# Kernel tuning notes

Hardware: AMD Instinct MI355X
Metric: run time of the kernel (lower is better)

Reference implementation:

```python
import jax, jax.numpy as jnp
import numpy as np

D_MODEL = 1024
N_HEADS = 16
D_K = D_MODEL // N_HEADS


def _xavier(key, shape):
    fan_in, fan_out = shape[1], shape[0]
    a = np.sqrt(6.0 / (fan_in + fan_out))
    return jax.random.uniform(key, shape, jnp.float32, -a, a)


def setup_inputs() -> dict:
    key = jax.random.key(0)
    kx, kq, kk, kv, ko = jax.random.split(key, 5)
    x = jax.random.normal(kx, (2, 2048, D_MODEL), jnp.float32)
    # nn.Linear weights are [out, in]; y = x @ W.T
    Wq = _xavier(kq, (D_MODEL, D_MODEL))
    Wk = _xavier(kk, (D_MODEL, D_MODEL))
    Wv = _xavier(kv, (D_MODEL, D_MODEL))
    Wo = _xavier(ko, (D_MODEL, D_MODEL))
    bo = jnp.zeros((D_MODEL,), jnp.float32)
    return {"x": x, "Wq": Wq, "Wk": Wk, "Wv": Wv, "Wo": Wo, "bo": bo}


def reference(x, Wq, Wk, Wv, Wo, bo):
    B, S, D = x.shape
    def split_heads(t):
        # [B,S,D] -> [B,H,S,d_k]
        return t.reshape(B, S, N_HEADS, D_K).transpose(0, 2, 1, 3)
    Q = split_heads(x @ Wq.T)
    K = split_heads(x @ Wk.T)
    V = split_heads(x @ Wv.T)
    scale = 1.0 / jnp.sqrt(jnp.asarray(D_K, x.dtype))
    scores = jnp.einsum('bhqd,bhkd->bhqk', Q, K) * scale  # [B,H,S,S]
    attn = jax.nn.softmax(scores, axis=-1)
    out = jnp.einsum('bhqk,bhkd->bhqd', attn, V)  # [B,H,S,d_k]
    out = out.transpose(0, 2, 1, 3).reshape(B, S, D)  # merge heads
    return out @ Wo.T + bo
```

## Files before the change

kernel.cpp:

```cpp
#include <hip/hip_runtime.h>


typedef __attribute__((ext_vector_type(8))) short bf16x8;
typedef __attribute__((ext_vector_type(4))) short bf16x4;
typedef __attribute__((ext_vector_type(4))) float f32x4;
typedef __attribute__((ext_vector_type(2))) unsigned int u32x2;

#define GK 1024
#define SEQ 2048
#define NHEAD 16
#define DKD 64
#define PADW 72

#define MFMA32(a, b, c) __builtin_amdgcn_mfma_f32_16x16x32_bf16((a), (b), (c), 0, 0, 0)
#define MFMA16(a, b, c) __builtin_amdgcn_mfma_f32_16x16x16bf16_1k((a), (b), (c), 0, 0, 0)

#if __has_builtin(__builtin_amdgcn_exp2f)
#define EXP2(x) __builtin_amdgcn_exp2f(x)
#else
#define EXP2(x) exp2f(x)
#endif

#define QSCALE 0.18033688011f

static __device__ __forceinline__ unsigned short f2bf(float f) {
    unsigned int u = __float_as_uint(f);
    u += 0x7fffu + ((u >> 16) & 1u);
    return (unsigned short)(u >> 16);
}

static __device__ __forceinline__ unsigned int pack_bf2(float a, float b) {
    unsigned int ua = __float_as_uint(a) + 0x8000u;
    unsigned int ub = __float_as_uint(b) + 0x8000u;
    return __builtin_amdgcn_perm(ub, ua, 0x07060302u);
}

__global__ __launch_bounds__(256) void cast_all(const float* __restrict__ x,
                                                const float* __restrict__ wq,
                                                const float* __restrict__ wk,
                                                const float* __restrict__ wv,
                                                const float* __restrict__ wo,
                                                unsigned short* __restrict__ Xb,
                                                unsigned short* __restrict__ Wqkv,
                                                unsigned short* __restrict__ Wob) {
    const int bid = blockIdx.x;
    const float* src; unsigned short* dst; int off;
    if (bid < 4096)      { src = x;  dst = Xb;             off = bid; }
    else if (bid < 5120) { src = wq; dst = Wqkv;           off = bid - 4096; }
    else if (bid < 6144) { src = wk; dst = Wqkv + 1048576; off = bid - 5120; }
    else if (bid < 7168) { src = wv; dst = Wqkv + 2097152; off = bid - 6144; }
    else                 { src = wo; dst = Wob;            off = bid - 7168; }
    const int i = off * 1024 + threadIdx.x * 4;
    float4 v = *(const float4*)(src + i);
    u32x2 p; p.x = pack_bf2(v.x, v.y); p.y = pack_bf2(v.z, v.w);
    *(u32x2*)(dst + i) = p;
}

template <int MODE, int BN>
__global__ __launch_bounds__(256) void gemm_bt(const unsigned short* __restrict__ A,
                                               const unsigned short* __restrict__ Bw,
                                               unsigned short* __restrict__ outb,
                                               float* __restrict__ outf,
                                               const float* __restrict__ bias) {
    constexpr int NJ = BN / 32;
    __shared__ __align__(16) unsigned short As[128 * 32];
    __shared__ __align__(16) unsigned short Bs[BN * 32];
    __shared__ __align__(16) unsigned short E[(MODE == 0) ? 4 * 64 * PADW : 4];

    const int t    = threadIdx.x;
    const int lane = t & 63;
    const int w    = t >> 6;
    const int wm   = (w >> 1) * 64;
    const int wn   = (w & 1) * (BN / 2);
    const int bm0  = blockIdx.x * 128;
    const int bn0  = blockIdx.y * BN;
    const int lm   = lane & 15;
    const int lq   = lane >> 4;
    const int kc   = lq * 8;

    const unsigned short* Ab = A + (size_t)bm0 * GK;
    const unsigned short* Bb = Bw + (size_t)bn0 * GK;

    f32x4 acc[4][NJ];
    const f32x4 Z4 = {0.f, 0.f, 0.f, 0.f};
#pragma unroll
    for (int i = 0; i < 4; i++)
#pragma unroll
        for (int j = 0; j < NJ; j++) acc[i][j] = Z4;

    const int q_uni = (t & ~63);

    for (int k0 = 0; k0 < GK; k0 += 32) {
        __syncthreads();
#pragma unroll
        for (int i = 0; i < 2; ++i) {
            int q = i * 256 + t;
            int r = q >> 2;
            int c = (q & 3) * 8;
            int q0 = i * 256 + q_uni;
            __builtin_amdgcn_global_load_lds(
                (const __attribute__((address_space(1))) void*)(Ab + (size_t)r * GK + k0 + c),
                (__attribute__((address_space(3))) void*)(As + (size_t)q0 * 8),
                16, 0, 0);
        }
#pragma unroll
        for (int i = 0; i < BN / 64; ++i) {
            int q = i * 256 + t;
            int r = q >> 2;
            int c = (q & 3) * 8;
            int q0 = i * 256 + q_uni;
            __builtin_amdgcn_global_load_lds(
                (const __attribute__((address_space(1))) void*)(Bb + (size_t)r * GK + k0 + c),
                (__attribute__((address_space(3))) void*)(Bs + (size_t)q0 * 8),
                16, 0, 0);
        }
        __syncthreads();

        bf16x8 af[4], bf[NJ];
#pragma unroll
        for (int i = 0; i < 4; i++)
            af[i] = *(const bf16x8*)(As + (wm + i * 16 + lm) * 32 + kc);
#pragma unroll
        for (int j = 0; j < NJ; j++)
            bf[j] = *(const bf16x8*)(Bs + (wn + j * 16 + lm) * 32 + kc);
#pragma unroll
        for (int i = 0; i < 4; i++)
#pragma unroll
            for (int j = 0; j < NJ; j++)
                acc[i][j] = MFMA32(af[i], bf[j], acc[i][j]);
    }

    if (MODE == 0) {
        unsigned short* Ew = E + w * (64 * PADW);
        const int nbase = bn0 + wn;
        const int which = nbase >> 10;
        const int hh    = (nbase & 1023) >> 6;
        if (which != 2) {
            const float sc = (which == 0) ? QSCALE : 1.0f;
#pragma unroll
            for (int i = 0; i < 4; i++)
#pragma unroll
                for (int j = 0; j < 4; j++)
#pragma unroll
                    for (int r = 0; r < 4; r++)
                        Ew[(i * 16 + lq * 4 + r) * PADW + j * 16 + lm] =
                            f2bf(acc[i][j][r] * sc);
            unsigned short* dst = outb + (size_t)which * 4194304;
#pragma unroll
            for (int rep = 0; rep < 8; ++rep) {
                const int mm = rep * 8 + (lane >> 3);
                const int d0 = (lane & 7) * 8;
                uint4 v = *(const uint4*)(Ew + mm * PADW + d0);
                const int m_g = bm0 + wm + mm;
                const int b = m_g >> 11, s = m_g & 2047;
                *(uint4*)(dst + (((size_t)(b * NHEAD + hh)) * SEQ + s) * DKD + d0) = v;
            }
        } else {
#pragma unroll
            for (int i = 0; i < 4; i++)
#pragma unroll
                for (int j = 0; j < 4; j++) {
                    u32x2 pk;
                    pk.x = pack_bf2(acc[i][j][0], acc[i][j][1]);
                    pk.y = pack_bf2(acc[i][j][2], acc[i][j][3]);
                    *(u32x2*)(Ew + (j * 16 + lm) * PADW + i * 16 + lq * 4) = pk;
                }
            unsigned short* dst = outb + (size_t)2 * 4194304;
#pragma unroll
            for (int rep = 0; rep < 8; ++rep) {
                const int nn = rep * 8 + (lane >> 3);
                const int mc = (lane & 7) * 8;
                uint4 v = *(const uint4*)(Ew + nn * PADW + mc);
                const int m_g = bm0 + wm + mc;
                const int b = m_g >> 11, s0 = m_g & 2047;
                *(uint4*)(dst + (((size_t)(b * NHEAD + hh)) * DKD + nn) * SEQ + s0) = v;
            }
        }
    } else {
#pragma unroll
        for (int i = 0; i < 4; i++) {
            const int mbase = bm0 + wm + i * 16 + lq * 4;
#pragma unroll
            for (int j = 0; j < NJ; j++) {
                const int n = bn0 + wn + j * 16 + lm;
#pragma unroll
                for (int r = 0; r < 4; r++)
                    outf[(size_t)(mbase + r) * 1024 + n] = acc[i][j][r] + bias[n];
            }
        }
    }
}

__global__ __launch_bounds__(256, 3) void attn_kernel(const unsigned short* __restrict__ Qg,
                                                      const unsigned short* __restrict__ Kg,
                                                      const unsigned short* __restrict__ Vtg,
                                                      unsigned short* __restrict__ Og) {
    __shared__ __align__(16) unsigned short KV[2][2][64 * PADW];

    const int id  = blockIdx.x;
    const int xcd = id & 7;
    const int j8  = id >> 3;
    const int bh  = xcd * 4 + (j8 & 3);
    const int qb  = j8 >> 2;
    const unsigned short* Qp  = Qg  + ((size_t)bh * SEQ + qb * 64) * DKD;
    const unsigned short* Kp  = Kg  + (size_t)bh * SEQ * DKD;
    const unsigned short* Vtp = Vtg + (size_t)bh * DKD * SEQ;

    const int t    = threadIdx.x;
    const int lane = t & 63;
    const int w    = t >> 6;
    const int lm   = lane & 15;
    const int kq   = lane >> 4;

    const f32x4 Z4 = {0.f, 0.f, 0.f, 0.f};

    bf16x8 aq[4][2];
#pragma unroll
    for (int c = 0; c < 4; ++c)
#pragma unroll
        for (int kk = 0; kk < 2; ++kk)
            aq[c][kk] = *(const bf16x8*)(Qp + (size_t)(c * 16 + lm) * DKD + kk * 32 + kq * 8);

    f32x4 o[4][4];
    float ls[4];
#pragma unroll
    for (int c = 0; c < 4; ++c) {
        ls[c] = 0.f;
#pragma unroll
        for (int dj = 0; dj < 4; ++dj) o[c][dj] = Z4;
    }

    const int sr = t >> 2, sc = (t & 3) * 16;
    uint4 kreg0, kreg1, vreg0, vreg1;
    {
        const unsigned short* kp = Kp + (size_t)sr * DKD + sc;
        const unsigned short* vp = Vtp + (size_t)sr * SEQ + sc;
        uint4 a0 = *(const uint4*)(kp), a1 = *(const uint4*)(kp + 8);
        uint4 b0 = *(const uint4*)(vp), b1 = *(const uint4*)(vp + 8);
        uint4* dk = (uint4*)(&KV[0][0][sr * PADW + sc]); dk[0] = a0; dk[1] = a1;
        uint4* dv = (uint4*)(&KV[0][1][sr * PADW + sc]); dv[0] = b0; dv[1] = b1;
    }
    {
        const unsigned short* kp = Kp + (size_t)(64 + sr) * DKD + sc;
        kreg0 = *(const uint4*)(kp); kreg1 = *(const uint4*)(kp + 8);
        const unsigned short* vp = Vtp + (size_t)sr * SEQ + 64 + sc;
        vreg0 = *(const uint4*)(vp); vreg1 = *(const uint4*)(vp + 8);
    }

    for (int kt = 0; kt < 32; ++kt) {
        __syncthreads();
        if (kt + 1 < 32) {
            uint4* dk = (uint4*)(&KV[(kt + 1) & 1][0][sr * PADW + sc]);
            dk[0] = kreg0; dk[1] = kreg1;
            uint4* dv = (uint4*)(&KV[(kt + 1) & 1][1][sr * PADW + sc]);
            dv[0] = vreg0; dv[1] = vreg1;
        }
        if (kt + 2 < 32) {
            const unsigned short* kp = Kp + (size_t)((kt + 2) * 64 + sr) * DKD + sc;
            kreg0 = *(const uint4*)(kp); kreg1 = *(const uint4*)(kp + 8);
            const unsigned short* vp = Vtp + (size_t)sr * SEQ + (kt + 2) * 64 + sc;
            vreg0 = *(const uint4*)(vp); vreg1 = *(const uint4*)(vp + 8);
        }
        const unsigned short* Kc = &KV[kt & 1][0][0];
        const unsigned short* Vc = &KV[kt & 1][1][0];

        bf16x8 ak0 = *(const bf16x8*)(Kc + (w * 16 + lm) * PADW + kq * 8);
        bf16x8 ak1 = *(const bf16x8*)(Kc + (w * 16 + lm) * PADW + 32 + kq * 8);
        f32x4 s[4];
#pragma unroll
        for (int c = 0; c < 4; ++c) {
            s[c] = MFMA32(ak0, aq[c][0], Z4);
            s[c] = MFMA32(ak1, aq[c][1], s[c]);
        }

#pragma unroll
        for (int c = 0; c < 4; ++c) {
#pragma unroll
            for (int r = 0; r < 4; ++r) s[c][r] = EXP2(s[c][r]);
            ls[c] += (s[c][0] + s[c][1]) + (s[c][2] + s[c][3]);
        }

        bf16x4 ap[4];
#pragma unroll
        for (int c = 0; c < 4; ++c) {
            u32x2 pk;
            pk.x = pack_bf2(s[c][0], s[c][1]);
            pk.y = pack_bf2(s[c][2], s[c][3]);
            ap[c] = __builtin_bit_cast(bf16x4, pk);
        }

#pragma unroll
        for (int dj = 0; dj < 4; ++dj) {
            bf16x4 bv = *(const bf16x4*)(Vc + (dj * 16 + lm) * PADW + w * 16 + kq * 4);
#pragma unroll
            for (int c = 0; c < 4; ++c)
                o[c][dj] = MFMA16(ap[c], bv, o[c][dj]);
        }
    }

    __syncthreads();
    float* Lf = (float*)(&KV[0][0][0]);

#pragma unroll
    for (int c = 0; c < 4; ++c) {
        float v = ls[c];
        v += __shfl_xor(v, 16);
        v += __shfl_xor(v, 32);
        if (kq == 0) Lf[w * 64 + c * 16 + lm] = v;
    }
    __syncthreads();

    const int rq = t >> 2;
    const int dq = (t & 3) * 8;
    float li = (Lf[rq] + Lf[64 + rq]) + (Lf[128 + rq] + Lf[192 + rq]);
#if __has_builtin(__builtin_amdgcn_rcpf)
    li = __builtin_amdgcn_rcpf(li);
#else
    li = 1.0f / li;
#endif
    __syncthreads();

    const int b = bh >> 4, h = bh & 15;
#pragma unroll
    for (int p = 0; p < 2; ++p) {
#pragma unroll
        for (int c = 0; c < 4; ++c)
#pragma unroll
            for (int djh = 0; djh < 2; ++djh) {
                const int dj = 2 * p + djh;
#pragma unroll
                for (int r = 0; r < 4; ++r)
                    Lf[(w * 64 + c * 16 + kq * 4 + r) * 36 + djh * 16 + lm] = o[c][dj][r];
            }
        __syncthreads();
        f32x4 a0 = Z4, a1 = Z4;
#pragma unroll
        for (int wp = 0; wp < 4; ++wp) {
            a0 += *(const f32x4*)(Lf + (wp * 64 + rq) * 36 + dq);
            a1 += *(const f32x4*)(Lf + (wp * 64 + rq) * 36 + dq + 4);
        }
        uint4 outv;
        outv.x = pack_bf2(a0[0] * li, a0[1] * li);
        outv.y = pack_bf2(a0[2] * li, a0[3] * li);
        outv.z = pack_bf2(a1[0] * li, a1[1] * li);
        outv.w = pack_bf2(a1[2] * li, a1[3] * li);
        *(uint4*)(Og + (((size_t)(b * SEQ + qb * 64 + rq)) * NHEAD + h) * DKD + p * 32 + dq) = outv;
        __syncthreads();
    }
}

extern "C" void kernel_launch(void* const* d_in, const int* in_sizes, int n_in,
                              void* d_out, int out_size, void* d_ws, size_t ws_size,
                              hipStream_t stream) {
    const float* x  = (const float*)d_in[0];
    const float* Wq = (const float*)d_in[1];
    const float* Wk = (const float*)d_in[2];
    const float* Wv = (const float*)d_in[3];
    const float* Wo = (const float*)d_in[4];
    const float* bo = (const float*)d_in[5];
    float* out = (float*)d_out;

    unsigned short* ws = (unsigned short*)d_ws;
    unsigned short* Xb   = ws;
    unsigned short* Wqkv = ws + 4194304;
    unsigned short* Wob  = ws + 7340032;
    unsigned short* QKV  = ws + 8388608;
    unsigned short* Ob   = ws + 20971520;

    cast_all<<<8192, 256, 0, stream>>>(x, Wq, Wk, Wv, Wo, Xb, Wqkv, Wob);
    gemm_bt<0, 128><<<dim3(32, 24), 256, 0, stream>>>(Xb, Wqkv, QKV, nullptr, nullptr);
    attn_kernel<<<1024, 256, 0, stream>>>(QKV, QKV + 4194304, QKV + 8388608, Ob);
    gemm_bt<1, 64><<<dim3(32, 16), 256, 0, stream>>>(Ob, Wob, nullptr, out, bo);
}
```

Baseline: 197.9 us.

## Double GEMM K-tile to 64 with XOR-swizzled LDS layout and aliased epilogue buffer

The GEMM main loop now stages a K-tile of 64 instead of 32, halving the number of barrier pairs per output tile. Global-to-LDS copies write columns in an XOR-swizzled order, and the fragment reads undo the swizzle, which is meant to avoid LDS bank conflicts on the wider rows. The epilogue staging buffer for MODE 0 now shares the same shared-memory block as the loop tiles, behind an extra barrier, to limit total LDS use. The larger tiles still raise LDS per block and may reduce occupancy.

```diff
diff --git a/kernel.cpp b/kernel.cpp
--- a/kernel.cpp
+++ b/kernel.cpp
@@ -63,9 +63,14 @@
                                                float* __restrict__ outf,
                                                const float* __restrict__ bias) {
     constexpr int NJ = BN / 32;
-    __shared__ __align__(16) unsigned short As[128 * 32];
-    __shared__ __align__(16) unsigned short Bs[BN * 32];
-    __shared__ __align__(16) unsigned short E[(MODE == 0) ? 4 * 64 * PADW : 4];
+    constexpr int LOOP_BYTES = 128 * 64 * 2 + BN * 64 * 2;
+    constexpr int EPI_BYTES  = 4 * 64 * PADW * 2;
+    constexpr int SMEM_BYTES = (MODE == 0)
+        ? (LOOP_BYTES > EPI_BYTES ? LOOP_BYTES : EPI_BYTES)
+        : LOOP_BYTES;
+    __shared__ __align__(16) unsigned char SMEM[SMEM_BYTES];
+    unsigned short* As = (unsigned short*)SMEM;
+    unsigned short* Bs = As + 128 * 64;
 
     const int t    = threadIdx.x;
     const int lane = t & 63;
@@ -76,7 +81,7 @@
     const int bn0  = blockIdx.y * BN;
     const int lm   = lane & 15;
     const int lq   = lane >> 4;
-    const int kc   = lq * 8;
+    const int swzb = lm & 7;
 
     const unsigned short* Ab = A + (size_t)bm0 * GK;
     const unsigned short* Bb = Bw + (size_t)bn0 * GK;
@@ -90,47 +95,53 @@
 
     const int q_uni = (t & ~63);
 
-    for (int k0 = 0; k0 < GK; k0 += 32) {
-        __syncthreads();
-#pragma unroll
-        for (int i = 0; i < 2; ++i) {
-            int q = i * 256 + t;
-            int r = q >> 2;
-            int c = (q & 3) * 8;
+    for (int k0 = 0; k0 < GK; k0 += 64) {
+        __syncthreads();
+#pragma unroll
+        for (int i = 0; i < 4; ++i) {
+            int q  = i * 256 + t;
+            int r  = q >> 3;
+            int gc = (q & 7) ^ (r & 7);
             int q0 = i * 256 + q_uni;
             __builtin_amdgcn_global_load_lds(
-                (const __attribute__((address_space(1))) void*)(Ab + (size_t)r * GK + k0 + c),
+                (const __attribute__((address_space(1))) void*)(Ab + (size_t)r * GK + k0 + gc * 8),
                 (__attribute__((address_space(3))) void*)(As + (size_t)q0 * 8),
                 16, 0, 0);
         }
 #pragma unroll
-        for (int i = 0; i < BN / 64; ++i) {
-            int q = i * 256 + t;
-            int r = q >> 2;
-            int c = (q & 3) * 8;
+        for (int i = 0; i < BN / 32; ++i) {
+            int q  = i * 256 + t;
+            int r  = q >> 3;
+            int gc = (q & 7) ^ (r & 7);
             int q0 = i * 256 + q_uni;
             __builtin_amdgcn_global_load_lds(
-                (const __attribute__((address_space(1))) void*)(Bb + (size_t)r * GK + k0 + c),
+                (const __attribute__((address_space(1))) void*)(Bb + (size_t)r * GK + k0 + gc * 8),
                 (__attribute__((address_space(3))) void*)(Bs + (size_t)q0 * 8),
                 16, 0, 0);
         }
         __syncthreads();
 
-        bf16x8 af[4], bf[NJ];
-#pragma unroll
-        for (int i = 0; i < 4; i++)
-            af[i] = *(const bf16x8*)(As + (wm + i * 16 + lm) * 32 + kc);
-#pragma unroll
-        for (int j = 0; j < NJ; j++)
-            bf[j] = *(const bf16x8*)(Bs + (wn + j * 16 + lm) * 32 + kc);
-#pragma unroll
-        for (int i = 0; i < 4; i++)
+#pragma unroll
+        for (int kk = 0; kk < 2; ++kk) {
+            const int swz = ((kk * 4 + lq) ^ swzb) * 8;
+            bf16x8 af[4], bf[NJ];
+#pragma unroll
+            for (int i = 0; i < 4; i++)
+                af[i] = *(const bf16x8*)(As + (wm + i * 16 + lm) * 64 + swz);
 #pragma unroll
             for (int j = 0; j < NJ; j++)
-                acc[i][j] = MFMA32(af[i], bf[j], acc[i][j]);
+                bf[j] = *(const bf16x8*)(Bs + (wn + j * 16 + lm) * 64 + swz);
+#pragma unroll
+            for (int i = 0; i < 4; i++)
+#pragma unroll
+                for (int j = 0; j < NJ; j++)
+                    acc[i][j] = MFMA32(af[i], bf[j], acc[i][j]);
+        }
     }
 
     if (MODE == 0) {
+        __syncthreads();
+        unsigned short* E  = (unsigned short*)SMEM;
         unsigned short* Ew = E + w * (64 * PADW);
         const int nbase = bn0 + wn;
         const int which = nbase >> 10;
```

Result: faster. 190.5 us (-3.7%).
